# Kernel tuning notes

Measured on AMD Instinct MI355X. Metric: run time of the kernel, lower is better.

## Reference

```python
import jax, jax.numpy as jnp
import numpy as np

N_USERS = 50000
N_ITEMS = 50000
N_NODES = N_USERS + N_ITEMS
NNZ = 1600000
EMB = 64
N_LAYERS = 3
REG = 1e-5
BATCH = 4096


def setup_inputs() -> dict:
    key = jax.random.key(0)
    ks = jax.random.split(key, 12)
    s = 1.0 / np.sqrt(EMB)
    return {
        "user_emb": jax.random.normal(ks[0], (N_USERS, EMB), jnp.float32) * s,
        "item_emb": jax.random.normal(ks[1], (N_ITEMS, EMB), jnp.float32) * s,
        "W_gc": jax.random.normal(ks[2], (N_LAYERS, EMB, EMB), jnp.float32) * s,
        "b_gc": jax.random.normal(ks[3], (N_LAYERS, 1, EMB), jnp.float32) * s,
        "W_bi": jax.random.normal(ks[4], (N_LAYERS, EMB, EMB), jnp.float32) * s,
        "b_bi": jax.random.normal(ks[5], (N_LAYERS, 1, EMB), jnp.float32) * s,
        "adj_val": jax.random.uniform(ks[6], (NNZ,), jnp.float32),
        "adj_row": jax.random.randint(ks[7], (NNZ,), 0, N_NODES, jnp.int32),
        "adj_col": jax.random.randint(ks[8], (NNZ,), 0, N_NODES, jnp.int32),
        "u": jax.random.randint(ks[9], (BATCH,), 0, N_USERS, jnp.int32),
        "i": jax.random.randint(ks[10], (BATCH,), 0, N_ITEMS, jnp.int32),
        "j": jax.random.randint(ks[11], (BATCH,), 0, N_ITEMS, jnp.int32),
    }


def _spmm(row, col, val, x):
    # sparse COO matmul: out[r] += val_e * x[col_e]
    return jax.ops.segment_sum(val[:, None] * x[col], row, num_segments=N_NODES)


def reference(user_emb, item_emb, W_gc, b_gc, W_bi, b_bi, adj_val,
              adj_row, adj_col, u, i, j):
    ego = jnp.concatenate([user_emb, item_emb], axis=0)  # [N, 64]
    all_embeddings = [ego]
    for k in range(N_LAYERS):
        side = _spmm(adj_row, adj_col, adj_val, ego)        # A @ ego
        side_L = side - ego                                  # (A - I) @ ego
        sum_emb = side @ W_gc[k] + b_gc[k]
        bi_emb = (ego * side_L) @ W_bi[k] + b_bi[k]
        ego = jax.nn.leaky_relu(sum_emb + bi_emb, negative_slope=0.01)
        # F.normalize(p=2, dim=1), eps=1e-12
        norm = jnp.linalg.norm(ego, axis=1, keepdims=True)
        all_embeddings.append(ego / jnp.maximum(norm, 1e-12))
    all_emb = jnp.concatenate(all_embeddings, axis=1)       # [N, 64*(1+3)]
    u_g, i_g = all_emb[:N_USERS], all_emb[N_USERS:]
    u_emb = u_g[u]
    p_emb = i_g[i]
    n_emb = i_g[j]
    y_ui = jnp.sum(u_emb * p_emb, axis=1)
    y_uj = jnp.sum(u_emb * n_emb, axis=1)
    log_prob = jnp.mean(jax.nn.log_sigmoid(y_ui - y_uj))
    bpr_loss = -log_prob
    l2norm = (jnp.sum(u_emb ** 2) / 2.0 + jnp.sum(p_emb ** 2) / 2.0
              + jnp.sum(n_emb ** 2) / 2.0) / u_emb.shape[0]
    return bpr_loss + REG * l2norm
```

## Files before the change

kernel.cpp:

```cpp
#include <hip/hip_runtime.h>
#include <math.h>

#define N_USERS 50000
#define N_ITEMS 50000
#define N_NODES 100000
#define NNZ_E   1600000
#define EMB     64
#define BATCH   4096
#define REG_C   1e-5f

#define BSH    8
#define NBUCK  ((N_NODES + 255) >> BSH)
#define BCAP   5120
#define NSB    256
#define CHUNK  ((NNZ_E + NSB - 1) / NSB)

#define LNB    256
#define LSPB   (BATCH / LNB)

__device__ __forceinline__ unsigned short f2bf(float f) {
    unsigned u = __float_as_uint(f);
    u = (u + 0x7FFFu + ((u >> 16) & 1u)) >> 16;
    return (unsigned short)u;
}
__device__ __forceinline__ float bf2f(unsigned short h) {
    return __uint_as_float(((unsigned)h) << 16);
}

__global__ __launch_bounds__(256) void init_ego(const float* __restrict__ ue,
                                                const float* __restrict__ ie,
                                                unsigned short* __restrict__ ego16) {
    const int total = N_NODES * EMB / 4;
    const int uf4   = N_USERS * EMB / 4;
    for (int idx = blockIdx.x * blockDim.x + threadIdx.x; idx < total;
         idx += gridDim.x * blockDim.x) {
        float4 v = (idx < uf4) ? ((const float4*)ue)[idx]
                               : ((const float4*)ie)[idx - uf4];
        ushort4 h;
        h.x = f2bf(v.x); h.y = f2bf(v.y); h.z = f2bf(v.z); h.w = f2bf(v.w);
        *(ushort4*)&ego16[(size_t)idx * 4] = h;
    }
}

__global__ __launch_bounds__(256) void binscatter(const int* __restrict__ rw,
                                                  const int* __restrict__ cl,
                                                  const float* __restrict__ val,
                                                  int* __restrict__ bcnt,
                                                  int2* __restrict__ bin) {
    __shared__ int lcount[NBUCK];
    __shared__ int lbase[NBUCK];
    const int t    = threadIdx.x;
    const int eend = min(NNZ_E, (int)((blockIdx.x + 1) * CHUNK));

    for (int b = t; b < NBUCK; b += 256) lcount[b] = 0;
    __syncthreads();

    for (int e = blockIdx.x * CHUNK + t; e < eend; e += 256)
        atomicAdd(&lcount[rw[e] >> BSH], 1);
    __syncthreads();

    for (int b = t; b < NBUCK; b += 256) {
        const int c = lcount[b];
        lbase[b]  = (c > 0) ? atomicAdd(&bcnt[b], c) : 0;
        lcount[b] = 0;
    }
    __syncthreads();

    for (int e = blockIdx.x * CHUNK + t; e < eend; e += 256) {
        const int r = rw[e];
        const int b = r >> BSH;
        const int ofs = atomicAdd(&lcount[b], 1);
        const int rel = lbase[b] + ofs;
        if (rel < BCAP)
            bin[(size_t)b * BCAP + rel] =
                make_int2(((r & 255) << 17) | cl[e], __float_as_int(val[e]));
    }
}

__global__ __launch_bounds__(512) void scan_buckets(const int* __restrict__ bcnt,
                                                    int* __restrict__ bbase) {
    const int t = threadIdx.x;
    const int lane = t & 63, w = t >> 6;
    const int v = (t < NBUCK) ? bcnt[t] : 0;
    int incl = v;
    #pragma unroll
    for (int off = 1; off < 64; off <<= 1) {
        const int x = __shfl_up(incl, off);
        if (lane >= off) incl += x;
    }
    __shared__ int wt[8];
    if (lane == 63) wt[w] = incl;
    __syncthreads();
    int wb = 0;
    #pragma unroll
    for (int q = 0; q < 8; ++q) wb += (q < w) ? wt[q] : 0;
    if (t < NBUCK) bbase[t] = wb + incl - v;
}

__global__ __launch_bounds__(256) void colsort_place(const int* __restrict__ bcnt,
                                                     int2* __restrict__ bin) {
    __shared__ int2 ebuf[BCAP];
    __shared__ int  cnt[256];
    __shared__ int  wt[4];
    const int t    = threadIdx.x;
    const int buck = blockIdx.x;
    const int n    = min(bcnt[buck], BCAP);
    int2* mybin = bin + (size_t)buck * BCAP;

    cnt[t] = 0;
    for (int i = t; i < n; i += 256) ebuf[i] = mybin[i];
    __syncthreads();

    for (int i = t; i < n; i += 256)
        atomicAdd(&cnt[(ebuf[i].x & 0x1FFFF) >> 9], 1);
    __syncthreads();

    const int c    = cnt[t];
    const int lane = t & 63, w = t >> 6;
    int incl = c;
    #pragma unroll
    for (int off = 1; off < 64; off <<= 1) {
        const int v = __shfl_up(incl, off);
        if (lane >= off) incl += v;
    }
    if (lane == 63) wt[w] = incl;
    __syncthreads();
    int wb = 0;
    #pragma unroll
    for (int q = 0; q < 4; ++q) wb += (q < w) ? wt[q] : 0;
    cnt[t] = wb + incl - c;
    __syncthreads();

    for (int i = t; i < n; i += 256) {
        const int2 e   = ebuf[i];
        const int  pos = atomicAdd(&cnt[(e.x & 0x1FFFF) >> 9], 1);
        mybin[pos] = e;
    }
}

__global__ __launch_bounds__(256) void csr_place(const int* __restrict__ bcnt,
                                                 const int* __restrict__ bbase,
                                                 const int2* __restrict__ bin,
                                                 int* __restrict__ row_ptr,
                                                 int2* __restrict__ ep) {
    __shared__ int rcnt[256];
    __shared__ int rbase[256];
    __shared__ int wt[4];
    const int t    = threadIdx.x;
    const int buck = blockIdx.x;
    const int n    = min(bcnt[buck], BCAP);
    const int base = bbase[buck];
    const int2* mybin = bin + (size_t)buck * BCAP;

    rcnt[t] = 0;
    __syncthreads();
    for (int i = t; i < n; i += 256)
        atomicAdd(&rcnt[mybin[i].x >> 17], 1);
    __syncthreads();

    const int c = rcnt[t];
    const int lane = t & 63, w = t >> 6;
    int incl = c;
    #pragma unroll
    for (int off = 1; off < 64; off <<= 1) {
        const int x = __shfl_up(incl, off);
        if (lane >= off) incl += x;
    }
    if (lane == 63) wt[w] = incl;
    __syncthreads();
    int wb = 0;
    #pragma unroll
    for (int q = 0; q < 4; ++q) wb += (q < w) ? wt[q] : 0;
    const int myb = base + wb + incl - c;

    const int gr = (buck << BSH) + t;
    if (gr < N_NODES) row_ptr[gr] = myb;
    if (buck == 0 && t == 0) row_ptr[N_NODES] = NNZ_E;
    rbase[t] = myb;
    __syncthreads();
    rcnt[t] = 0;
    __syncthreads();

    for (int i = t; i < n; i += 256) {
        const int2 e  = mybin[i];
        const int r8  = e.x >> 17;
        const int col = e.x & 0x1FFFF;
        const int ofs = atomicAdd(&rcnt[r8], 1);
        ep[rbase[r8] + ofs] = make_int2(col, e.y);
    }
}

__global__ __launch_bounds__(256) void spmm_csr(const int* __restrict__ rp,
                                                const int2* __restrict__ ep,
                                                const unsigned short* __restrict__ xb,
                                                unsigned short* __restrict__ y16) {
    const int w    = (blockIdx.x * blockDim.x + threadIdx.x) >> 6;
    const int l    = threadIdx.x & 63;
    const int sub  = l & 31;
    const int half = l >> 5;
    if (w >= N_NODES) return;
    const int beg = rp[w];
    const int end = rp[w + 1];
    float a0 = 0.f, a1 = 0.f;
    int e = beg;
    for (; e + 8 <= end; e += 8) {
        int2 p[4];
        #pragma unroll
        for (int q = 0; q < 4; ++q) p[q] = ep[e + 2 * q + half];
        unsigned xv[4];
        #pragma unroll
        for (int q = 0; q < 4; ++q)
            xv[q] = *(const unsigned*)&xb[((size_t)p[q].x << 6) + (sub << 1)];
        #pragma unroll
        for (int q = 0; q < 4; ++q) {
            const float v = __int_as_float(p[q].y);
            a0 += v * __uint_as_float(xv[q] << 16);
            a1 += v * __uint_as_float(xv[q] & 0xFFFF0000u);
        }
    }
    for (; e + 2 <= end; e += 2) {
        const int2 pq = ep[e + half];
        const unsigned xv = *(const unsigned*)&xb[((size_t)pq.x << 6) + (sub << 1)];
        const float v = __int_as_float(pq.y);
        a0 += v * __uint_as_float(xv << 16);
        a1 += v * __uint_as_float(xv & 0xFFFF0000u);
    }
    if (e < end) {
        const int2 pq = ep[e];
        const unsigned xv = *(const unsigned*)&xb[((size_t)pq.x << 6) + (sub << 1)];
        const float v = half ? 0.f : __int_as_float(pq.y);
        a0 += v * __uint_as_float(xv << 16);
        a1 += v * __uint_as_float(xv & 0xFFFF0000u);
    }
    a0 += __shfl_xor(a0, 32);
    a1 += __shfl_xor(a1, 32);
    if (half == 0) {
        const unsigned outp = (unsigned)f2bf(a0) | ((unsigned)f2bf(a1) << 16);
        ((unsigned*)y16)[((size_t)w << 5) + sub] = outp;
    }
}

__global__ __launch_bounds__(512) void layer_update(const unsigned short* __restrict__ side16,
                                                    unsigned short* __restrict__ ego16,
                                                    const float* __restrict__ Wgc,
                                                    const float* __restrict__ bgc,
                                                    const float* __restrict__ Wbi,
                                                    const float* __restrict__ bbi) {
    __shared__ float HT[EMB * EMB];
    __shared__ float GT[EMB * EMB];
    __shared__ float WG[EMB * EMB];
    __shared__ float WB[EMB * EMB];

    const int t  = threadIdx.x;
    const int r0 = blockIdx.x * 64;

    #pragma unroll
    for (int it = 0; it < 2; ++it) {
        const int f4  = t + it * 512;
        const int d   = f4 >> 4;
        const int c0  = (f4 & 15) * 4;

        float4 wg = ((const float4*)Wgc)[f4];
        float4 wb = ((const float4*)Wbi)[f4];
        *(float4*)&WG[d * EMB + c0] = wg;
        *(float4*)&WB[d * EMB + c0] = wb;

        const int gr = r0 + d;
        float hv[4] = {0.f, 0.f, 0.f, 0.f};
        float ev[4] = {0.f, 0.f, 0.f, 0.f};
        if (gr < N_NODES) {
            const ushort4 s4h = *(const ushort4*)&side16[(size_t)gr * EMB + c0];
            const ushort4 e4h = *(const ushort4*)&ego16[(size_t)gr * EMB + c0];
            hv[0] = bf2f(s4h.x); hv[1] = bf2f(s4h.y); hv[2] = bf2f(s4h.z); hv[3] = bf2f(s4h.w);
            ev[0] = bf2f(e4h.x); ev[1] = bf2f(e4h.y); ev[2] = bf2f(e4h.z); ev[3] = bf2f(e4h.w);
        }
        #pragma unroll
        for (int q = 0; q < 4; ++q) {
            const int dd = c0 + q;
            const int sw = (dd & 7) << 2;
            HT[dd * EMB + (d ^ sw)] = hv[q];
            GT[dd * EMB + (d ^ sw)] = ev[q] * (hv[q] - ev[q]);
        }
    }
    __syncthreads();

    const int tr = t >> 5;
    const int to = t & 31;

    float acc[4][2];
    #pragma unroll
    for (int i2 = 0; i2 < 4; ++i2) { acc[i2][0] = 0.f; acc[i2][1] = 0.f; }

    #pragma unroll 8
    for (int d = 0; d < EMB; ++d) {
        const int sw = (d & 7) << 2;
        const float4 ah4 = *(const float4*)&HT[d * EMB + ((tr * 4) ^ sw)];
        const float4 ag4 = *(const float4*)&GT[d * EMB + ((tr * 4) ^ sw)];
        const float2 wg2 = *(const float2*)&WG[d * EMB + to * 2];
        const float2 wb2 = *(const float2*)&WB[d * EMB + to * 2];
        const float ah[4] = {ah4.x, ah4.y, ah4.z, ah4.w};
        const float ag[4] = {ag4.x, ag4.y, ag4.z, ag4.w};
        #pragma unroll
        for (int i2 = 0; i2 < 4; ++i2) {
            acc[i2][0] += ah[i2] * wg2.x + ag[i2] * wb2.x;
            acc[i2][1] += ah[i2] * wg2.y + ag[i2] * wb2.y;
        }
    }

    const float2 bg2 = *(const float2*)&bgc[to * 2];
    const float2 bb2 = *(const float2*)&bbi[to * 2];
    const float bs0 = bg2.x + bb2.x;
    const float bs1 = bg2.y + bb2.y;

    #pragma unroll
    for (int i2 = 0; i2 < 4; ++i2) {
        const int gr = r0 + tr * 4 + i2;
        if (gr < N_NODES) {
            float v0 = acc[i2][0] + bs0;
            float v1 = acc[i2][1] + bs1;
            v0 = (v0 >= 0.f) ? v0 : 0.01f * v0;
            v1 = (v1 >= 0.f) ? v1 : 0.01f * v1;
            const unsigned outp = (unsigned)f2bf(v0) | ((unsigned)f2bf(v1) << 16);
            ((unsigned*)ego16)[(size_t)gr * 32 + to] = outp;
        }
    }
}

__global__ __launch_bounds__(256) void gather_norm(const unsigned short* __restrict__ ego16,
                                                   const int* __restrict__ u,
                                                   const int* __restrict__ ii,
                                                   const int* __restrict__ jj,
                                                   float* __restrict__ Gk) {
    const int gtid = blockIdx.x * blockDim.x + threadIdx.x;
    const int wave = gtid >> 6;
    const int lane = threadIdx.x & 63;
    if (wave >= 3 * BATCH) return;
    const int a = wave / BATCH;
    const int b = wave - a * BATCH;
    const int node = (a == 0) ? u[b] : N_USERS + ((a == 1) ? ii[b] : jj[b]);
    const float v = bf2f(ego16[(size_t)node * EMB + lane]);
    float ss = v * v;
    #pragma unroll
    for (int m = 32; m; m >>= 1) ss += __shfl_xor(ss, m);
    const float inv = 1.f / fmaxf(sqrtf(ss), 1e-12f);
    Gk[(size_t)wave * EMB + lane] = v * inv;
}

__global__ __launch_bounds__(256) void loss_partial(const float* __restrict__ ue,
                                                    const float* __restrict__ ie,
                                                    const float* __restrict__ G,
                                                    const int* __restrict__ u,
                                                    const int* __restrict__ ii,
                                                    const int* __restrict__ jj,
                                                    float* __restrict__ partial) {
    __shared__ float wsum[4];
    const int t    = threadIdx.x;
    const int lane = t & 63;
    const int w    = t >> 6;

    float sum = 0.f;
    #pragma unroll
    for (int s = 0; s < LSPB / 4; ++s) {
        const int b = blockIdx.x * LSPB + w * (LSPB / 4) + s;
        const int uu = u[b], pi = ii[b], nj = jj[b];
        float uv[4], pv[4], nv[4];
        uv[0] = ue[(size_t)uu * EMB + lane];
        pv[0] = ie[(size_t)pi * EMB + lane];
        nv[0] = ie[(size_t)nj * EMB + lane];
        #pragma unroll
        for (int k = 0; k < 3; ++k) {
            uv[k + 1] = G[(((size_t)k * 3 + 0) * BATCH + b) * EMB + lane];
            pv[k + 1] = G[(((size_t)k * 3 + 1) * BATCH + b) * EMB + lane];
            nv[k + 1] = G[(((size_t)k * 3 + 2) * BATCH + b) * EMB + lane];
        }
        float yui = 0.f, yuj = 0.f, l2 = 0.f;
        #pragma unroll
        for (int q = 0; q < 4; ++q) {
            yui += uv[q] * pv[q];
            yuj += uv[q] * nv[q];
            l2  += uv[q] * uv[q] + pv[q] * pv[q] + nv[q] * nv[q];
        }
        #pragma unroll
        for (int m = 32; m; m >>= 1) {
            yui += __shfl_xor(yui, m);
            yuj += __shfl_xor(yuj, m);
            l2  += __shfl_xor(l2, m);
        }
        const float d  = yui - yuj;
        const float sp = (d > 0.f) ? log1pf(expf(-d)) : (-d + log1pf(expf(d)));
        sum += sp * (1.f / BATCH) + REG_C * (l2 * 0.5f) * (1.f / BATCH);
    }
    if (lane == 0) wsum[w] = sum;
    __syncthreads();
    if (t == 0) partial[blockIdx.x] = wsum[0] + wsum[1] + wsum[2] + wsum[3];
}

__global__ __launch_bounds__(256) void final_reduce(const float* __restrict__ partial,
                                                    float* __restrict__ out) {
    __shared__ float wsum[4];
    const int t = threadIdx.x;
    const int lane = t & 63, w = t >> 6;
    float v = partial[t];
    #pragma unroll
    for (int m = 32; m; m >>= 1) v += __shfl_xor(v, m);
    if (lane == 0) wsum[w] = v;
    __syncthreads();
    if (t == 0) out[0] = wsum[0] + wsum[1] + wsum[2] + wsum[3];
}

extern "C" void kernel_launch(void* const* d_in, const int* in_sizes, int n_in,
                              void* d_out, int out_size, void* d_ws, size_t ws_size,
                              hipStream_t stream) {
    const float* ue   = (const float*)d_in[0];
    const float* ie   = (const float*)d_in[1];
    const float* Wgc  = (const float*)d_in[2];
    const float* bgc  = (const float*)d_in[3];
    const float* Wbi  = (const float*)d_in[4];
    const float* bbi  = (const float*)d_in[5];
    const float* aval = (const float*)d_in[6];
    const int*   arow = (const int*)d_in[7];
    const int*   acol = (const int*)d_in[8];
    const int*   u    = (const int*)d_in[9];
    const int*   ii   = (const int*)d_in[10];
    const int*   jj   = (const int*)d_in[11];
    float* out = (float*)d_out;

    const size_t NE = (size_t)N_NODES * EMB;
    char* p = (char*)d_ws;
    unsigned short* ego16  = (unsigned short*)p;  p += NE * 2;
    unsigned short* side16 = (unsigned short*)p;  p += NE * 2;
    float* G     = (float*)p;                 p += (size_t)9 * BATCH * EMB * 4;
    float* lpart = (float*)p;                 p += (size_t)LNB * 4;
    int* row_ptr = (int*)p;                   p += (size_t)(N_NODES + 2) * 4;
    int* bcnt    = (int*)p;                   p += (size_t)(NBUCK + 1) * 4;
    int* bbase   = (int*)p;                   p += (size_t)(NBUCK + 1) * 4;
    p = (char*)(((uintptr_t)p + 15) & ~(uintptr_t)15);
    int2* epack  = (int2*)p;                  p += (size_t)NNZ_E * 8;
    int2* bin    = (int2*)p;                  p += (size_t)NBUCK * BCAP * 8;

    hipMemsetAsync(bcnt, 0, (NBUCK + 1) * sizeof(int), stream);
    hipLaunchKernelGGL(binscatter, dim3(NSB), dim3(256), 0, stream,
                       arow, acol, aval, bcnt, bin);
    hipLaunchKernelGGL(scan_buckets, dim3(1), dim3(512), 0, stream, bcnt, bbase);
    hipLaunchKernelGGL(colsort_place, dim3(NBUCK), dim3(256), 0, stream,
                       bcnt, bin);
    hipLaunchKernelGGL(csr_place, dim3(NBUCK), dim3(256), 0, stream,
                       bcnt, bbase, bin, row_ptr, epack);

    hipLaunchKernelGGL(init_ego, dim3(2048), dim3(256), 0, stream, ue, ie, ego16);

    for (int k = 0; k < 3; ++k) {
        hipLaunchKernelGGL(spmm_csr, dim3((N_NODES * 64 + 255) / 256), dim3(256), 0, stream,
                           row_ptr, epack, ego16, side16);
        hipLaunchKernelGGL(layer_update, dim3((N_NODES + 63) / 64), dim3(512), 0, stream,
                           side16, ego16,
                           Wgc + (size_t)k * EMB * EMB, bgc + (size_t)k * EMB,
                           Wbi + (size_t)k * EMB * EMB, bbi + (size_t)k * EMB);
        hipLaunchKernelGGL(gather_norm, dim3((3 * BATCH + 3) / 4), dim3(256), 0, stream,
                           ego16, u, ii, jj, G + (size_t)k * 3 * BATCH * EMB);
    }

    hipLaunchKernelGGL(loss_partial, dim3(LNB), dim3(256), 0, stream,
                       ue, ie, G, u, ii, jj, lpart);
    hipLaunchKernelGGL(final_reduce, dim3(1), dim3(256), 0, stream, lpart, out);
}
```

Measured before the change: 466.6 us.

## Fuse SpMM into layer update and merge CSR build kernels into one

Folds the bucket scan, column sort and CSR placement into a single sort_place kernel. Each block computes its base offset from the preceding bucket counts, and the column sort permutes shared-memory indices instead of rewriting the bin. SpMM is fused into the dense layer-update kernel: each wave computes 8 rows of A@ego directly into shared-memory tiles, stored as bf16 to save LDS, and ego ping-pongs between two buffers. This removes the side buffer round-trip through global memory and several launches. In exchange, SpMM parallelism drops to one block per 64 rows with serial per-wave row loops, and the intermediate tiles carry bf16 rounding.

New measurement: 586.5 us. +25.7%, slower.

```diff
diff --git a/kernel.cpp b/kernel.cpp
--- a/kernel.cpp
+++ b/kernel.cpp
@@ -77,177 +77,103 @@
     }
 }
 
-__global__ __launch_bounds__(512) void scan_buckets(const int* __restrict__ bcnt,
-                                                    int* __restrict__ bbase) {
-    const int t = threadIdx.x;
-    const int lane = t & 63, w = t >> 6;
-    const int v = (t < NBUCK) ? bcnt[t] : 0;
-    int incl = v;
-    #pragma unroll
-    for (int off = 1; off < 64; off <<= 1) {
-        const int x = __shfl_up(incl, off);
-        if (lane >= off) incl += x;
-    }
-    __shared__ int wt[8];
-    if (lane == 63) wt[w] = incl;
-    __syncthreads();
-    int wb = 0;
-    #pragma unroll
-    for (int q = 0; q < 8; ++q) wb += (q < w) ? wt[q] : 0;
-    if (t < NBUCK) bbase[t] = wb + incl - v;
-}
-
-__global__ __launch_bounds__(256) void colsort_place(const int* __restrict__ bcnt,
-                                                     int2* __restrict__ bin) {
+__global__ __launch_bounds__(256) void sort_place(const int* __restrict__ bcnt,
+                                                  const int2* __restrict__ bin,
+                                                  int* __restrict__ row_ptr,
+                                                  int2* __restrict__ ep) {
     __shared__ int2 ebuf[BCAP];
-    __shared__ int  cnt[256];
-    __shared__ int  wt[4];
-    const int t    = threadIdx.x;
-    const int buck = blockIdx.x;
-    const int n    = min(bcnt[buck], BCAP);
-    int2* mybin = bin + (size_t)buck * BCAP;
-
-    cnt[t] = 0;
-    for (int i = t; i < n; i += 256) ebuf[i] = mybin[i];
-    __syncthreads();
-
-    for (int i = t; i < n; i += 256)
-        atomicAdd(&cnt[(ebuf[i].x & 0x1FFFF) >> 9], 1);
-    __syncthreads();
-
-    const int c    = cnt[t];
-    const int lane = t & 63, w = t >> 6;
-    int incl = c;
-    #pragma unroll
-    for (int off = 1; off < 64; off <<= 1) {
-        const int v = __shfl_up(incl, off);
-        if (lane >= off) incl += v;
-    }
-    if (lane == 63) wt[w] = incl;
-    __syncthreads();
-    int wb = 0;
-    #pragma unroll
-    for (int q = 0; q < 4; ++q) wb += (q < w) ? wt[q] : 0;
-    cnt[t] = wb + incl - c;
-    __syncthreads();
-
-    for (int i = t; i < n; i += 256) {
-        const int2 e   = ebuf[i];
-        const int  pos = atomicAdd(&cnt[(e.x & 0x1FFFF) >> 9], 1);
-        mybin[pos] = e;
-    }
-}
-
-__global__ __launch_bounds__(256) void csr_place(const int* __restrict__ bcnt,
-                                                 const int* __restrict__ bbase,
-                                                 const int2* __restrict__ bin,
-                                                 int* __restrict__ row_ptr,
-                                                 int2* __restrict__ ep) {
+    __shared__ unsigned short sidx[BCAP];
+    __shared__ int cnt[256];
     __shared__ int rcnt[256];
     __shared__ int rbase[256];
     __shared__ int wt[4];
+    __shared__ int sbase;
     const int t    = threadIdx.x;
     const int buck = blockIdx.x;
+    const int lane = t & 63, w = t >> 6;
     const int n    = min(bcnt[buck], BCAP);
-    const int base = bbase[buck];
-    const int2* mybin = bin + (size_t)buck * BCAP;
-
+
+    int ps = 0;
+    for (int j = t; j < buck; j += 256) ps += min(bcnt[j], BCAP);
+    #pragma unroll
+    for (int m = 32; m; m >>= 1) ps += __shfl_xor(ps, m);
+    if (lane == 0) wt[w] = ps;
+    cnt[t]  = 0;
     rcnt[t] = 0;
     __syncthreads();
+    if (t == 0) sbase = wt[0] + wt[1] + wt[2] + wt[3];
+    for (int i = t; i < n; i += 256) ebuf[i] = bin[(size_t)buck * BCAP + i];
+    __syncthreads();
+
     for (int i = t; i < n; i += 256)
-        atomicAdd(&rcnt[mybin[i].x >> 17], 1);
-    __syncthreads();
-
-    const int c = rcnt[t];
-    const int lane = t & 63, w = t >> 6;
-    int incl = c;
-    #pragma unroll
-    for (int off = 1; off < 64; off <<= 1) {
-        const int x = __shfl_up(incl, off);
-        if (lane >= off) incl += x;
-    }
-    if (lane == 63) wt[w] = incl;
-    __syncthreads();
-    int wb = 0;
-    #pragma unroll
-    for (int q = 0; q < 4; ++q) wb += (q < w) ? wt[q] : 0;
-    const int myb = base + wb + incl - c;
-
-    const int gr = (buck << BSH) + t;
-    if (gr < N_NODES) row_ptr[gr] = myb;
-    if (buck == 0 && t == 0) row_ptr[N_NODES] = NNZ_E;
-    rbase[t] = myb;
-    __syncthreads();
-    rcnt[t] = 0;
+        atomicAdd(&cnt[(ebuf[i].x & 0x1FFFF) >> 9], 1);
+    __syncthreads();
+
+    {
+        const int c = cnt[t];
+        int incl = c;
+        #pragma unroll
+        for (int off = 1; off < 64; off <<= 1) {
+            const int v = __shfl_up(incl, off);
+            if (lane >= off) incl += v;
+        }
+        if (lane == 63) wt[w] = incl;
+        __syncthreads();
+        int wb = 0;
+        #pragma unroll
+        for (int q = 0; q < 4; ++q) wb += (q < w) ? wt[q] : 0;
+        cnt[t] = wb + incl - c;
+    }
     __syncthreads();
 
     for (int i = t; i < n; i += 256) {
-        const int2 e  = mybin[i];
+        const int pos = atomicAdd(&cnt[(ebuf[i].x & 0x1FFFF) >> 9], 1);
+        sidx[pos] = (unsigned short)i;
+    }
+    for (int i = t; i < n; i += 256)
+        atomicAdd(&rcnt[ebuf[i].x >> 17], 1);
+    __syncthreads();
+
+    {
+        const int c2 = rcnt[t];
+        int incl = c2;
+        #pragma unroll
+        for (int off = 1; off < 64; off <<= 1) {
+            const int v = __shfl_up(incl, off);
+            if (lane >= off) incl += v;
+        }
+        if (lane == 63) wt[w] = incl;
+        __syncthreads();
+        int wb = 0;
+        #pragma unroll
+        for (int q = 0; q < 4; ++q) wb += (q < w) ? wt[q] : 0;
+        const int myb = sbase + wb + incl - c2;
+        rbase[t] = myb;
+        const int gr = (buck << BSH) + t;
+        if (gr < N_NODES) row_ptr[gr] = myb;
+        if (buck == NBUCK - 1 && t == 0) row_ptr[N_NODES] = sbase + n;
+        rcnt[t] = 0;
+    }
+    __syncthreads();
+
+    for (int k = t; k < n; k += 256) {
+        const int2 e  = ebuf[sidx[k]];
         const int r8  = e.x >> 17;
-        const int col = e.x & 0x1FFFF;
         const int ofs = atomicAdd(&rcnt[r8], 1);
-        ep[rbase[r8] + ofs] = make_int2(col, e.y);
-    }
-}
-
-__global__ __launch_bounds__(256) void spmm_csr(const int* __restrict__ rp,
-                                                const int2* __restrict__ ep,
-                                                const unsigned short* __restrict__ xb,
-                                                unsigned short* __restrict__ y16) {
-    const int w    = (blockIdx.x * blockDim.x + threadIdx.x) >> 6;
-    const int l    = threadIdx.x & 63;
-    const int sub  = l & 31;
-    const int half = l >> 5;
-    if (w >= N_NODES) return;
-    const int beg = rp[w];
-    const int end = rp[w + 1];
-    float a0 = 0.f, a1 = 0.f;
-    int e = beg;
-    for (; e + 8 <= end; e += 8) {
-        int2 p[4];
-        #pragma unroll
-        for (int q = 0; q < 4; ++q) p[q] = ep[e + 2 * q + half];
-        unsigned xv[4];
-        #pragma unroll
-        for (int q = 0; q < 4; ++q)
-            xv[q] = *(const unsigned*)&xb[((size_t)p[q].x << 6) + (sub << 1)];
-        #pragma unroll
-        for (int q = 0; q < 4; ++q) {
-            const float v = __int_as_float(p[q].y);
-            a0 += v * __uint_as_float(xv[q] << 16);
-            a1 += v * __uint_as_float(xv[q] & 0xFFFF0000u);
-        }
-    }
-    for (; e + 2 <= end; e += 2) {
-        const int2 pq = ep[e + half];
-        const unsigned xv = *(const unsigned*)&xb[((size_t)pq.x << 6) + (sub << 1)];
-        const float v = __int_as_float(pq.y);
-        a0 += v * __uint_as_float(xv << 16);
-        a1 += v * __uint_as_float(xv & 0xFFFF0000u);
-    }
-    if (e < end) {
-        const int2 pq = ep[e];
-        const unsigned xv = *(const unsigned*)&xb[((size_t)pq.x << 6) + (sub << 1)];
-        const float v = half ? 0.f : __int_as_float(pq.y);
-        a0 += v * __uint_as_float(xv << 16);
-        a1 += v * __uint_as_float(xv & 0xFFFF0000u);
-    }
-    a0 += __shfl_xor(a0, 32);
-    a1 += __shfl_xor(a1, 32);
-    if (half == 0) {
-        const unsigned outp = (unsigned)f2bf(a0) | ((unsigned)f2bf(a1) << 16);
-        ((unsigned*)y16)[((size_t)w << 5) + sub] = outp;
-    }
-}
-
-__global__ __launch_bounds__(512) void layer_update(const unsigned short* __restrict__ side16,
-                                                    unsigned short* __restrict__ ego16,
-                                                    const float* __restrict__ Wgc,
-                                                    const float* __restrict__ bgc,
-                                                    const float* __restrict__ Wbi,
-                                                    const float* __restrict__ bbi) {
-    __shared__ float HT[EMB * EMB];
-    __shared__ float GT[EMB * EMB];
+        ep[rbase[r8] + ofs] = make_int2(e.x & 0x1FFFF, e.y);
+    }
+}
+
+__global__ __launch_bounds__(512) void spmm_layer(const int* __restrict__ rp,
+                                                  const int2* __restrict__ ep,
+                                                  const unsigned short* __restrict__ xin,
+                                                  unsigned short* __restrict__ xout,
+                                                  const float* __restrict__ Wgc,
+                                                  const float* __restrict__ bgc,
+                                                  const float* __restrict__ Wbi,
+                                                  const float* __restrict__ bbi) {
+    __shared__ unsigned short HT[EMB * EMB];
+    __shared__ unsigned short GT[EMB * EMB];
     __shared__ float WG[EMB * EMB];
     __shared__ float WB[EMB * EMB];
 
@@ -256,37 +182,66 @@
 
     #pragma unroll
     for (int it = 0; it < 2; ++it) {
-        const int f4  = t + it * 512;
-        const int d   = f4 >> 4;
-        const int c0  = (f4 & 15) * 4;
-
-        float4 wg = ((const float4*)Wgc)[f4];
-        float4 wb = ((const float4*)Wbi)[f4];
-        *(float4*)&WG[d * EMB + c0] = wg;
-        *(float4*)&WB[d * EMB + c0] = wb;
-
-        const int gr = r0 + d;
-        float hv[4] = {0.f, 0.f, 0.f, 0.f};
-        float ev[4] = {0.f, 0.f, 0.f, 0.f};
-        if (gr < N_NODES) {
-            const ushort4 s4h = *(const ushort4*)&side16[(size_t)gr * EMB + c0];
-            const ushort4 e4h = *(const ushort4*)&ego16[(size_t)gr * EMB + c0];
-            hv[0] = bf2f(s4h.x); hv[1] = bf2f(s4h.y); hv[2] = bf2f(s4h.z); hv[3] = bf2f(s4h.w);
-            ev[0] = bf2f(e4h.x); ev[1] = bf2f(e4h.y); ev[2] = bf2f(e4h.z); ev[3] = bf2f(e4h.w);
-        }
-        #pragma unroll
-        for (int q = 0; q < 4; ++q) {
-            const int dd = c0 + q;
-            const int sw = (dd & 7) << 2;
-            HT[dd * EMB + (d ^ sw)] = hv[q];
-            GT[dd * EMB + (d ^ sw)] = ev[q] * (hv[q] - ev[q]);
-        }
+        const int f4 = t + it * 512;
+        const int d  = f4 >> 4, c0 = (f4 & 15) * 4;
+        *(float4*)&WG[d * EMB + c0] = ((const float4*)Wgc)[f4];
+        *(float4*)&WB[d * EMB + c0] = ((const float4*)Wbi)[f4];
+    }
+
+    const int w = t >> 6, l = t & 63, sub = l & 31, half = l >> 5;
+    #pragma unroll 1
+    for (int q = 0; q < 8; ++q) {
+        const int rl = w * 8 + q;
+        const int r  = r0 + rl;
+        float a0 = 0.f, a1 = 0.f;
+        if (r < N_NODES) {
+            const int beg = rp[r], end = rp[r + 1];
+            int e = beg;
+            for (; e + 8 <= end; e += 8) {
+                int2 p[4];
+                #pragma unroll
+                for (int z = 0; z < 4; ++z) p[z] = ep[e + 2 * z + half];
+                unsigned xv[4];
+                #pragma unroll
+                for (int z = 0; z < 4; ++z)
+                    xv[z] = *(const unsigned*)&xin[((size_t)p[z].x << 6) + (sub << 1)];
+                #pragma unroll
+                for (int z = 0; z < 4; ++z) {
+                    const float v = __int_as_float(p[z].y);
+                    a0 += v * __uint_as_float(xv[z] << 16);
+                    a1 += v * __uint_as_float(xv[z] & 0xFFFF0000u);
+                }
+            }
+            for (; e + 2 <= end; e += 2) {
+                const int2 pq = ep[e + half];
+                const unsigned xv = *(const unsigned*)&xin[((size_t)pq.x << 6) + (sub << 1)];
+                const float v = __int_as_float(pq.y);
+                a0 += v * __uint_as_float(xv << 16);
+                a1 += v * __uint_as_float(xv & 0xFFFF0000u);
+            }
+            if (e < end) {
+                const int2 pq = ep[e];
+                const unsigned xv = *(const unsigned*)&xin[((size_t)pq.x << 6) + (sub << 1)];
+                const float v = half ? 0.f : __int_as_float(pq.y);
+                a0 += v * __uint_as_float(xv << 16);
+                a1 += v * __uint_as_float(xv & 0xFFFF0000u);
+            }
+        }
+        a0 += __shfl_xor(a0, 32);
+        a1 += __shfl_xor(a1, 32);
+        const int dd = (sub << 1) + half;
+        const float h = half ? a1 : a0;
+        float ev = 0.f;
+        if (r < N_NODES) ev = bf2f(xin[((size_t)r << 6) + dd]);
+        const float g  = ev * (h - ev);
+        const int sw = (dd & 7) << 2;
+        HT[dd * EMB + (rl ^ sw)] = f2bf(h);
+        GT[dd * EMB + (rl ^ sw)] = f2bf(g);
     }
     __syncthreads();
 
     const int tr = t >> 5;
     const int to = t & 31;
-
     float acc[4][2];
     #pragma unroll
     for (int i2 = 0; i2 < 4; ++i2) { acc[i2][0] = 0.f; acc[i2][1] = 0.f; }
@@ -294,12 +249,12 @@
     #pragma unroll 8
     for (int d = 0; d < EMB; ++d) {
         const int sw = (d & 7) << 2;
-        const float4 ah4 = *(const float4*)&HT[d * EMB + ((tr * 4) ^ sw)];
-        const float4 ag4 = *(const float4*)&GT[d * EMB + ((tr * 4) ^ sw)];
+        const ushort4 ah4 = *(const ushort4*)&HT[d * EMB + ((tr * 4) ^ sw)];
+        const ushort4 ag4 = *(const ushort4*)&GT[d * EMB + ((tr * 4) ^ sw)];
         const float2 wg2 = *(const float2*)&WG[d * EMB + to * 2];
         const float2 wb2 = *(const float2*)&WB[d * EMB + to * 2];
-        const float ah[4] = {ah4.x, ah4.y, ah4.z, ah4.w};
-        const float ag[4] = {ag4.x, ag4.y, ag4.z, ag4.w};
+        const float ah[4] = {bf2f(ah4.x), bf2f(ah4.y), bf2f(ah4.z), bf2f(ah4.w)};
+        const float ag[4] = {bf2f(ag4.x), bf2f(ag4.y), bf2f(ag4.z), bf2f(ag4.w)};
         #pragma unroll
         for (int i2 = 0; i2 < 4; ++i2) {
             acc[i2][0] += ah[i2] * wg2.x + ag[i2] * wb2.x;
@@ -321,7 +276,7 @@
             v0 = (v0 >= 0.f) ? v0 : 0.01f * v0;
             v1 = (v1 >= 0.f) ? v1 : 0.01f * v1;
             const unsigned outp = (unsigned)f2bf(v0) | ((unsigned)f2bf(v1) << 16);
-            ((unsigned*)ego16)[(size_t)gr * 32 + to] = outp;
+            ((unsigned*)xout)[(size_t)gr * 32 + to] = outp;
         }
     }
 }
@@ -427,13 +382,12 @@
 
     const size_t NE = (size_t)N_NODES * EMB;
     char* p = (char*)d_ws;
-    unsigned short* ego16  = (unsigned short*)p;  p += NE * 2;
-    unsigned short* side16 = (unsigned short*)p;  p += NE * 2;
+    unsigned short* bufA = (unsigned short*)p;  p += NE * 2;
+    unsigned short* bufB = (unsigned short*)p;  p += NE * 2;
     float* G     = (float*)p;                 p += (size_t)9 * BATCH * EMB * 4;
     float* lpart = (float*)p;                 p += (size_t)LNB * 4;
     int* row_ptr = (int*)p;                   p += (size_t)(N_NODES + 2) * 4;
     int* bcnt    = (int*)p;                   p += (size_t)(NBUCK + 1) * 4;
-    int* bbase   = (int*)p;                   p += (size_t)(NBUCK + 1) * 4;
     p = (char*)(((uintptr_t)p + 15) & ~(uintptr_t)15);
     int2* epack  = (int2*)p;                  p += (size_t)NNZ_E * 8;
     int2* bin    = (int2*)p;                  p += (size_t)NBUCK * BCAP * 8;
@@ -441,23 +395,20 @@
     hipMemsetAsync(bcnt, 0, (NBUCK + 1) * sizeof(int), stream);
     hipLaunchKernelGGL(binscatter, dim3(NSB), dim3(256), 0, stream,
                        arow, acol, aval, bcnt, bin);
-    hipLaunchKernelGGL(scan_buckets, dim3(1), dim3(512), 0, stream, bcnt, bbase);
-    hipLaunchKernelGGL(colsort_place, dim3(NBUCK), dim3(256), 0, stream,
-                       bcnt, bin);
-    hipLaunchKernelGGL(csr_place, dim3(NBUCK), dim3(256), 0, stream,
-                       bcnt, bbase, bin, row_ptr, epack);
-
-    hipLaunchKernelGGL(init_ego, dim3(2048), dim3(256), 0, stream, ue, ie, ego16);
-
+    hipLaunchKernelGGL(sort_place, dim3(NBUCK), dim3(256), 0, stream,
+                       bcnt, bin, row_ptr, epack);
+
+    hipLaunchKernelGGL(init_ego, dim3(2048), dim3(256), 0, stream, ue, ie, bufA);
+
+    const unsigned short* inb[3]  = {bufA, bufB, bufA};
+    unsigned short*       outb[3] = {bufB, bufA, bufB};
     for (int k = 0; k < 3; ++k) {
-        hipLaunchKernelGGL(spmm_csr, dim3((N_NODES * 64 + 255) / 256), dim3(256), 0, stream,
-                           row_ptr, epack, ego16, side16);
-        hipLaunchKernelGGL(layer_update, dim3((N_NODES + 63) / 64), dim3(512), 0, stream,
-                           side16, ego16,
+        hipLaunchKernelGGL(spmm_layer, dim3((N_NODES + 63) / 64), dim3(512), 0, stream,
+                           row_ptr, epack, inb[k], outb[k],
                            Wgc + (size_t)k * EMB * EMB, bgc + (size_t)k * EMB,
                            Wbi + (size_t)k * EMB * EMB, bbi + (size_t)k * EMB);
         hipLaunchKernelGGL(gather_norm, dim3((3 * BATCH + 3) / 4), dim3(256), 0, stream,
-                           ego16, u, ii, jj, G + (size_t)k * 3 * BATCH * EMB);
+                           outb[k], u, ii, jj, G + (size_t)k * 3 * BATCH * EMB);
     }
 
     hipLaunchKernelGGL(loss_partial, dim3(LNB), dim3(256), 0, stream,
```
